# Kernel tuning notes

Hardware: AMD Instinct MI355X
Metric: run time of the kernel (lower is better)

The kernel has to match this reference:

```python
import jax, jax.numpy as jnp
import numpy as np

# Faithful distillation of AttentionNet's cross-modal attention block.
# The resnet50/PointNet backbones are replaced by their output feature maps
# (img: [B,256,64,64], pc2d: [B,2048,64,64]) supplied as inputs, since the
# kernel-relevant math is the conv1x1 projections + bmm/softmax/bmm attention,
# followed by global avg-pool, concat, and the fc + log_softmax head.
# Note: the original forward contains a bug (img_v1 overwritten by img.view)
# and dead code; we implement the clearly intended attention math.

B, CQ, CK, H, W = 16, 256, 2048, 64, 64
NUM_CLASS = 40


def conv1x1(x, w, b):
    # x: [B,Cin,H,W], w: [Cout,Cin], b: [Cout]
    return jnp.einsum('bchw,oc->bohw', x, w) + b[None, :, None, None]


def setup_inputs() -> dict:
    key = jax.random.key(0)
    ks = jax.random.split(key, 16)
    s = lambda fan_in: 1.0 / np.sqrt(fan_in)
    return {
        'img': jax.random.normal(ks[0], (B, CQ, H, W), jnp.float32),
        'pc2d': jax.random.normal(ks[1], (B, CK, H, W), jnp.float32),
        'Wq': jax.random.normal(ks[2], (CQ, CQ), jnp.float32) * s(CQ),
        'bq': jnp.zeros((CQ,), jnp.float32),
        'Wk': jax.random.normal(ks[3], (CQ, CK), jnp.float32) * s(CK),
        'bk': jnp.zeros((CQ,), jnp.float32),
        'Wvi': jax.random.normal(ks[4], (CQ, CQ), jnp.float32) * s(CQ),
        'bvi': jnp.zeros((CQ,), jnp.float32),
        'Wvp': jax.random.normal(ks[5], (CK, CK), jnp.float32) * s(CK),
        'bvp': jnp.zeros((CK,), jnp.float32),
        'gamma1': jnp.zeros((1,), jnp.float32),
        'W1': jax.random.normal(ks[6], (1024, CQ + CK), jnp.float32) * s(CQ + CK),
        'b1': jnp.zeros((1024,), jnp.float32),
        'W2': jax.random.normal(ks[7], (NUM_CLASS, 1024), jnp.float32) * s(1024),
        'b2': jnp.zeros((NUM_CLASS,), jnp.float32),
    }


def reference(img, pc2d, Wq, bq, Wk, bk, Wvi, bvi, Wvp, bvp, gamma1, W1, b1, W2, b2):
    N = H * W  # 4096
    q = conv1x1(img, Wq, bq).reshape(B, CQ, N).transpose(0, 2, 1)   # [B,N,256]
    k = conv1x1(pc2d, Wk, bk).reshape(B, CQ, N)                     # [B,256,N]
    att = jax.nn.softmax(jnp.einsum('bnc,bcm->bnm', q, k), axis=-1)  # [B,N,N]
    # image branch: out = gamma * bmm(V_img, att^T) + img
    vi = conv1x1(img, Wvi, bvi).reshape(B, CQ, N)
    img_att = jnp.einsum('bcn,bmn->bcm', vi, att).reshape(B, CQ, H, W)
    img_out = gamma1[0] * img_att + img
    # point-cloud branch: bmm(V_pc, att^T)
    vp = conv1x1(pc2d, Wvp, bvp).reshape(B, CK, N)
    pc_out = jnp.einsum('bcn,bmn->bcm', vp, att)                    # [B,2048,N]
    # global average pool + concat + MLP head with log_softmax
    img_feat = img_out.mean(axis=(2, 3))                            # [B,256]
    pc_feat = pc_out.mean(axis=2)                                   # [B,2048]
    fused = jnp.concatenate([img_feat, pc_feat], axis=-1)           # [B,2304]
    h = jax.nn.relu(fused @ W1.T + b1)
    logits = h @ W2.T + b2
    return jax.nn.log_softmax(logits, axis=1)
```

## Files before the change

### kernel.cpp

```cpp
#include <hip/hip_runtime.h>
#include <cstdint>

typedef __attribute__((ext_vector_type(8))) short short8;
typedef __attribute__((ext_vector_type(4))) float f32x4;

#define LOG2E 1.44269504088896340736f
#define SHIFT 64.0f

__device__ __forceinline__ unsigned short f2bf(float x) {
  union { float f; unsigned u; } c; c.f = x;
  unsigned r = c.u + 0x7fffu + ((c.u >> 16) & 1u);
  return (unsigned short)(r >> 16);
}

__device__ __forceinline__ void gl2lds16(const void* g, void* l) {
  __builtin_amdgcn_global_load_lds((const __attribute__((address_space(1))) void*)g,
                                   (__attribute__((address_space(3))) void*)l, 16, 0, 0);
}

__global__ void cvt_bf16(const float* __restrict__ src, unsigned short* __restrict__ dst, int n4) {
  int i = blockIdx.x * 256 + threadIdx.x;
  if (i >= n4) return;
  float4 v = ((const float4*)src)[i];
  ushort4 o;
  o.x = f2bf(v.x); o.y = f2bf(v.y); o.z = f2bf(v.z); o.w = f2bf(v.w);
  ((ushort4*)dst)[i] = o;
}

__device__ __forceinline__ void stage_resident(char* ldsbase, const char* src, int w, int lane) {
  const int p = lane & 31;
  const int rlo = lane >> 5;
#pragma unroll
  for (int it = 0; it < 16; ++it) {
    const int r = w * 32 + it * 2 + rlo;
    const int gs = (p & 24) | ((p & 7) ^ (r & 7));
    gl2lds16(src + (size_t)r * 512 + gs * 16, ldsbase + (w * 16 + it) * 1024);
  }
}

__device__ __forceinline__ void stage_stream(char* buf, const char* srcbase, int roff0, int roff1,
                                             int w) {
  gl2lds16(srcbase + roff0, buf + w * 1024);
  gl2lds16(srcbase + roff1, buf + 4096 + w * 1024);
}

__global__ __launch_bounds__(256, 2) void attn_rowsum(
    const unsigned short* __restrict__ qt, const unsigned short* __restrict__ kt,
    float* __restrict__ row_l) {
  extern __shared__ char pool[];
  const int b = blockIdx.y, i0 = blockIdx.x * 128;
  const int t = threadIdx.x, w = t >> 6, lane = t & 63, q = lane >> 4, ln = lane & 15;
  const int ihalf = w >> 1, jhalf = w & 1;
  const char* qres = (const char*)(qt + ((size_t)b * 4096 + i0) * 256);
  const char* kb = (const char*)(kt + (size_t)b * 4096 * 256);
  const int rr0 = w * 16 + (lane >> 2);
  const int gsS = (lane & 3) ^ ((lane >> 3) & 3);
  const int roff0 = rr0 * 512 + gsS * 16;
  const int roff1 = (64 + rr0) * 512 + gsS * 16;
  const int aRow = (ihalf * 64 + ln) * 512;
  const int bRow = jhalf * 4096 + ln * 64 + (q ^ ((ln >> 1) & 3)) * 16;
  float lacc[4][4] = {};

  stage_resident(pool, qres, w, lane);
  stage_stream(pool + 65536, kb, roff0, roff1, w);
  __syncthreads();

#pragma unroll 1
  for (int jt = 0; jt < 32; ++jt) {
    f32x4 acc[4][4] = {};
#pragma unroll
    for (int c = 0; c < 8; ++c) {
      const int s = jt * 8 + c;
      if (s + 1 < 256) {
        const int njt = (s + 1) >> 3, nc = (s + 1) & 7;
        stage_stream(pool + 65536 + ((s + 1) & 1) * 8192,
                     kb + (size_t)njt * 65536 + nc * 64, roff0, roff1, w);
      }
      const char* B = pool + 65536 + (s & 1) * 8192;
      const int posA = ((4 * c) & 24) | ((4 * (c & 1) + q) ^ (ln & 7));
      short8 af[4], bfr[4];
#pragma unroll
      for (int mt = 0; mt < 4; ++mt) af[mt] = *(const short8*)(pool + aRow + mt * 8192 + posA * 16);
#pragma unroll
      for (int nt = 0; nt < 4; ++nt) bfr[nt] = *(const short8*)(B + bRow + nt * 1024);
#pragma unroll
      for (int mt = 0; mt < 4; ++mt)
#pragma unroll
        for (int nt = 0; nt < 4; ++nt)
          acc[mt][nt] = __builtin_amdgcn_mfma_f32_16x16x32_bf16(af[mt], bfr[nt], acc[mt][nt], 0, 0, 0);
      __syncthreads();
    }
#pragma unroll
    for (int mt = 0; mt < 4; ++mt)
#pragma unroll
      for (int r = 0; r < 4; ++r) {
        float e = exp2f(acc[mt][0][r] * LOG2E - SHIFT) + exp2f(acc[mt][1][r] * LOG2E - SHIFT)
                + exp2f(acc[mt][2][r] * LOG2E - SHIFT) + exp2f(acc[mt][3][r] * LOG2E - SHIFT);
        e += __shfl_xor(e, 1); e += __shfl_xor(e, 2);
        e += __shfl_xor(e, 4); e += __shfl_xor(e, 8);
        lacc[mt][r] += e;
      }
  }
  float* lred = (float*)(pool + 65536);
  if (ln == 0) {
#pragma unroll
    for (int mt = 0; mt < 4; ++mt)
#pragma unroll
      for (int r = 0; r < 4; ++r)
        lred[jhalf * 128 + ihalf * 64 + mt * 16 + q * 4 + r] = lacc[mt][r];
  }
  __syncthreads();
  if (t < 128) row_l[b * 4096 + i0 + t] = lred[t] + lred[128 + t];
}

__global__ void inv_kernel(const float* __restrict__ l, float* __restrict__ linv) {
  int i = blockIdx.x * 256 + threadIdx.x;
  linv[i] = 1.0f / l[i];
}

__global__ __launch_bounds__(256, 2) void attn_colsum(
    const unsigned short* __restrict__ qt, const unsigned short* __restrict__ kt,
    const float* __restrict__ linv, float* __restrict__ s_col) {
  extern __shared__ char pool[];
  const int b = blockIdx.y, j0 = blockIdx.x * 128;
  const int t = threadIdx.x, w = t >> 6, lane = t & 63, q = lane >> 4, ln = lane & 15;
  const int ihalf = w >> 1, jhalf = w & 1;
  const char* kres = (const char*)(kt + ((size_t)b * 4096 + j0) * 256);
  const char* qb = (const char*)(qt + (size_t)b * 4096 * 256);
  const int rr0 = w * 16 + (lane >> 2);
  const int gsS = (lane & 3) ^ ((lane >> 3) & 3);
  const int roff0 = rr0 * 512 + gsS * 16;
  const int roff1 = (64 + rr0) * 512 + gsS * 16;
  const int aRow = ihalf * 4096 + ln * 64 + (q ^ ((ln >> 1) & 3)) * 16;
  const int bRow = (jhalf * 64 + ln) * 512;
  float scacc[4] = {};

  stage_resident(pool, kres, w, lane);
  stage_stream(pool + 65536, qb, roff0, roff1, w);
  __syncthreads();

#pragma unroll 1
  for (int it = 0; it < 32; ++it) {
    const float4* lp = (const float4*)(linv + (size_t)b * 4096 + it * 128 + ihalf * 64 + q * 4);
    float4 lv[4];
#pragma unroll
    for (int mt = 0; mt < 4; ++mt) lv[mt] = lp[mt * 4];

    f32x4 acc[4][4] = {};
#pragma unroll
    for (int c = 0; c < 8; ++c) {
      const int s = it * 8 + c;
      if (s + 1 < 256) {
        const int nit = (s + 1) >> 3, nc = (s + 1) & 7;
        stage_stream(pool + 65536 + ((s + 1) & 1) * 8192,
                     qb + (size_t)nit * 65536 + nc * 64, roff0, roff1, w);
      }
      const char* A = pool + 65536 + (s & 1) * 8192;
      const int posB = ((4 * c) & 24) | ((4 * (c & 1) + q) ^ (ln & 7));
      short8 af[4], bfr[4];
#pragma unroll
      for (int mt = 0; mt < 4; ++mt) af[mt] = *(const short8*)(A + aRow + mt * 1024);
#pragma unroll
      for (int nt = 0; nt < 4; ++nt) bfr[nt] = *(const short8*)(pool + bRow + nt * 8192 + posB * 16);
#pragma unroll
      for (int mt = 0; mt < 4; ++mt)
#pragma unroll
        for (int nt = 0; nt < 4; ++nt)
          acc[mt][nt] = __builtin_amdgcn_mfma_f32_16x16x32_bf16(af[mt], bfr[nt], acc[mt][nt], 0, 0, 0);
      __syncthreads();
    }
#pragma unroll
    for (int nt = 0; nt < 4; ++nt) {
      float v = 0.f;
#pragma unroll
      for (int mt = 0; mt < 4; ++mt) {
        v += exp2f(acc[mt][nt][0] * LOG2E - SHIFT) * lv[mt].x;
        v += exp2f(acc[mt][nt][1] * LOG2E - SHIFT) * lv[mt].y;
        v += exp2f(acc[mt][nt][2] * LOG2E - SHIFT) * lv[mt].z;
        v += exp2f(acc[mt][nt][3] * LOG2E - SHIFT) * lv[mt].w;
      }
      v += __shfl_xor(v, 16); v += __shfl_xor(v, 32);
      scacc[nt] += v;
    }
  }
  float* sred = (float*)(pool + 65536);
  if (q == 0) {
#pragma unroll
    for (int nt = 0; nt < 4; ++nt)
      sred[ihalf * 128 + jhalf * 64 + nt * 16 + ln] = scacc[nt];
  }
  __syncthreads();
  if (t < 128) s_col[b * 4096 + j0 + t] = sred[t] + sred[128 + t];
}

__global__ __launch_bounds__(256, 2) void proj_kernel(
    const float* __restrict__ In, const unsigned short* __restrict__ Wbf,
    const float* __restrict__ bias, unsigned short* __restrict__ Out, int Kdim) {
  __shared__ unsigned short Alds[64 * 72];
  __shared__ unsigned short Blds[256 * 72];
  const int b = blockIdx.y, sp0 = blockIdx.x * 64;
  const int t = threadIdx.x, w = t >> 6, lane = t & 63, q = lane >> 4, ln = lane & 15;
  f32x4 acc[4][4] = {};
  const int nch = Kdim >> 6;
  for (int ch = 0; ch < nch; ++ch) {
    const int ci0 = ch * 64;
#pragma unroll
    for (int p = 0; p < 8; ++p) {
      int s = t + 256 * p;
      int row = s >> 3, sl = s & 7;
      *(uint4*)(&Blds[row * 72 + sl * 8]) = *(const uint4*)(&Wbf[(size_t)row * Kdim + ci0 + sl * 8]);
    }
    {
      const int cp = t >> 3, spg = t & 7;
      const float* r0 = In + ((size_t)b * Kdim + ci0 + 2 * cp) * 4096 + sp0 + spg * 8;
      const float* r1 = r0 + 4096;
      float4 a0 = *(const float4*)(r0);
      float4 a1 = *(const float4*)(r0 + 4);
      float4 b0 = *(const float4*)(r1);
      float4 b1 = *(const float4*)(r1 + 4);
      float va[8] = {a0.x, a0.y, a0.z, a0.w, a1.x, a1.y, a1.z, a1.w};
      float vb[8] = {b0.x, b0.y, b0.z, b0.w, b1.x, b1.y, b1.z, b1.w};
#pragma unroll
      for (int k2 = 0; k2 < 8; ++k2) {
        unsigned u0 = f2bf(va[k2]), u1 = f2bf(vb[k2]);
        *(unsigned*)(&Alds[(spg * 8 + k2) * 72 + 2 * cp]) = u0 | (u1 << 16);
      }
    }
    __syncthreads();
#pragma unroll
    for (int ks = 0; ks < 2; ++ks) {
      short8 af[4], bfr[4];
#pragma unroll
      for (int mt = 0; mt < 4; ++mt)
        af[mt] = *(const short8*)(&Alds[(mt * 16 + ln) * 72 + ks * 32 + q * 8]);
#pragma unroll
      for (int nt = 0; nt < 4; ++nt)
        bfr[nt] = *(const short8*)(&Blds[(w * 64 + nt * 16 + ln) * 72 + ks * 32 + q * 8]);
#pragma unroll
      for (int mt = 0; mt < 4; ++mt)
#pragma unroll
        for (int nt = 0; nt < 4; ++nt)
          acc[mt][nt] = __builtin_amdgcn_mfma_f32_16x16x32_bf16(af[mt], bfr[nt], acc[mt][nt], 0, 0, 0);
    }
    __syncthreads();
  }
#pragma unroll
  for (int nt = 0; nt < 4; ++nt) {
    int co = w * 64 + nt * 16 + ln;
    float bv = bias[co];
#pragma unroll
    for (int mt = 0; mt < 4; ++mt)
#pragma unroll
      for (int r = 0; r < 4; ++r) {
        int sp = sp0 + mt * 16 + q * 4 + r;
        Out[((size_t)b * 4096 + sp) * 256 + co] = f2bf(acc[mt][nt][r] + bv);
      }
  }
}

__global__ void sbar_kernel(const float* __restrict__ s_col, float* __restrict__ sbar) {
  const int b = blockIdx.x, t = threadIdx.x;
  float v = 0.f;
  for (int k = 0; k < 16; ++k) v += s_col[b * 4096 + t + 256 * k];
  for (int m = 1; m < 64; m <<= 1) v += __shfl_xor(v, m);
  __shared__ float red[4];
  if ((t & 63) == 0) red[t >> 6] = v;
  __syncthreads();
  if (t == 0) sbar[b] = (red[0] + red[1] + red[2] + red[3]) * (1.f / 4096.f);
}

__global__ void pool_kernel(const float* __restrict__ img, const float* __restrict__ pc2d,
                            const float* __restrict__ s_col, float* __restrict__ u_pool,
                            float* __restrict__ imean, float* __restrict__ t_pool) {
  const int b = blockIdx.y, chunk = blockIdx.x;
  const int t = threadIdx.x, ch_l = t >> 2, j = t & 3;
  const bool isimg = chunk < 4;
  int ch;
  const float4* row4;
  if (isimg) {
    ch = chunk * 64 + ch_l;
    row4 = (const float4*)(img + ((size_t)b * 256 + ch) * 4096);
  } else {
    ch = (chunk - 4) * 64 + ch_l;
    row4 = (const float4*)(pc2d + ((size_t)b * 2048 + ch) * 4096);
  }
  const float4* s4 = (const float4*)(s_col + b * 4096);
  float accd = 0.f, accs = 0.f;
  for (int kk = 0; kk < 256; ++kk) {
    float4 x = row4[j + 4 * kk];
    float4 sv = s4[j + 4 * kk];
    accd += x.x * sv.x + x.y * sv.y + x.z * sv.z + x.w * sv.w;
    accs += x.x + x.y + x.z + x.w;
  }
  accd += __shfl_xor(accd, 1); accd += __shfl_xor(accd, 2);
  accs += __shfl_xor(accs, 1); accs += __shfl_xor(accs, 2);
  if (j == 0) {
    if (isimg) {
      u_pool[b * 256 + ch] = accd * (1.f / 4096.f);
      imean[b * 256 + ch] = accs * (1.f / 4096.f);
    } else {
      t_pool[b * 2048 + ch] = accd * (1.f / 4096.f);
    }
  }
}

__global__ void imgfeat_kernel(const float* __restrict__ Wvi, const float* __restrict__ bvi,
                               const float* __restrict__ gamma1, const float* __restrict__ u_pool,
                               const float* __restrict__ imean, const float* __restrict__ sbar,
                               float* __restrict__ fused) {
  const int t = threadIdx.x;
  const int co = blockIdx.x * 64 + (t >> 2), j = t & 3;
  float acc[16];
#pragma unroll
  for (int b = 0; b < 16; ++b) acc[b] = 0.f;
  const float4* w4 = (const float4*)(Wvi + (size_t)co * 256);
  for (int kk = 0; kk < 16; ++kk) {
    float4 wv = w4[j + 4 * kk];
#pragma unroll
    for (int b = 0; b < 16; ++b) {
      float4 uv = ((const float4*)(u_pool + b * 256))[j + 4 * kk];
      acc[b] += wv.x * uv.x + wv.y * uv.y + wv.z * uv.z + wv.w * uv.w;
    }
  }
#pragma unroll
  for (int b = 0; b < 16; ++b) { acc[b] += __shfl_xor(acc[b], 1); acc[b] += __shfl_xor(acc[b], 2); }
  if (j == 0) {
    float g = gamma1[0], bv = bvi[co];
#pragma unroll
    for (int b = 0; b < 16; ++b)
      fused[b * 2304 + co] = g * (acc[b] + bv * sbar[b]) + imean[b * 256 + co];
  }
}

__global__ void pcfeat_kernel(const float* __restrict__ Wvp, const float* __restrict__ bvp,
                              const float* __restrict__ t_pool, const float* __restrict__ sbar,
                              float* __restrict__ fused) {
  const int t = threadIdx.x;
  const int co = blockIdx.x * 64 + (t >> 2), j = t & 3;
  float acc[16];
#pragma unroll
  for (int b = 0; b < 16; ++b) acc[b] = 0.f;
  const float4* w4 = (const float4*)(Wvp + (size_t)co * 2048);
  for (int kk = 0; kk < 128; ++kk) {
    float4 wv = w4[j + 4 * kk];
#pragma unroll
    for (int b = 0; b < 16; ++b) {
      float4 tv = ((const float4*)(t_pool + b * 2048))[j + 4 * kk];
      acc[b] += wv.x * tv.x + wv.y * tv.y + wv.z * tv.z + wv.w * tv.w;
    }
  }
#pragma unroll
  for (int b = 0; b < 16; ++b) { acc[b] += __shfl_xor(acc[b], 1); acc[b] += __shfl_xor(acc[b], 2); }
  if (j == 0) {
    float bv = bvp[co];
#pragma unroll
    for (int b = 0; b < 16; ++b)
      fused[b * 2304 + 256 + co] = acc[b] + bv * sbar[b];
  }
}

__global__ void head1_kernel(const float* __restrict__ W1, const float* __restrict__ b1,
                             const float* __restrict__ fused, float* __restrict__ h) {
  const int t = threadIdx.x;
  const int o = blockIdx.x * 64 + (t >> 2), j = t & 3;
  float acc[16];
#pragma unroll
  for (int b = 0; b < 16; ++b) acc[b] = 0.f;
  const float4* w4 = (const float4*)(W1 + (size_t)o * 2304);
  for (int kk = 0; kk < 144; ++kk) {
    float4 wv = w4[j + 4 * kk];
#pragma unroll
    for (int b = 0; b < 16; ++b) {
      float4 fv = ((const float4*)(fused + b * 2304))[j + 4 * kk];
      acc[b] += wv.x * fv.x + wv.y * fv.y + wv.z * fv.z + wv.w * fv.w;
    }
  }
#pragma unroll
  for (int b = 0; b < 16; ++b) { acc[b] += __shfl_xor(acc[b], 1); acc[b] += __shfl_xor(acc[b], 2); }
  if (j == 0) {
    float bv = b1[o];
#pragma unroll
    for (int b = 0; b < 16; ++b) h[b * 1024 + o] = fmaxf(acc[b] + bv, 0.f);
  }
}

__global__ void head2_kernel(const float* __restrict__ W2, const float* __restrict__ b2,
                             const float* __restrict__ h, float* __restrict__ out) {
  const int b = blockIdx.x, t = threadIdx.x;
  __shared__ float logit[40];
  __shared__ float red[4];
  float4 hv = ((const float4*)(h + b * 1024))[t];
  for (int c = 0; c < 40; ++c) {
    float4 wv = ((const float4*)(W2 + (size_t)c * 1024))[t];
    float p = wv.x * hv.x + wv.y * hv.y + wv.z * hv.z + wv.w * hv.w;
    for (int m = 1; m < 64; m <<= 1) p += __shfl_xor(p, m);
    if ((t & 63) == 0) red[t >> 6] = p;
    __syncthreads();
    if (t == 0) logit[c] = red[0] + red[1] + red[2] + red[3] + b2[c];
    __syncthreads();
  }
  if (t == 0) {
    float mx = -1e30f;
    for (int c = 0; c < 40; ++c) mx = fmaxf(mx, logit[c]);
    float s = 0.f;
    for (int c = 0; c < 40; ++c) s += expf(logit[c] - mx);
    float ls = logf(s);
    for (int c = 0; c < 40; ++c) out[b * 40 + c] = logit[c] - mx - ls;
  }
}

extern "C" void kernel_launch(void* const* d_in, const int* in_sizes, int n_in,
                              void* d_out, int out_size, void* d_ws, size_t ws_size,
                              hipStream_t stream) {
  (void)in_sizes; (void)n_in; (void)out_size; (void)ws_size;
  const float* img    = (const float*)d_in[0];
  const float* pc2d   = (const float*)d_in[1];
  const float* Wq     = (const float*)d_in[2];
  const float* bq     = (const float*)d_in[3];
  const float* Wk     = (const float*)d_in[4];
  const float* bk     = (const float*)d_in[5];
  const float* Wvi    = (const float*)d_in[6];
  const float* bvi    = (const float*)d_in[7];
  const float* Wvp    = (const float*)d_in[8];
  const float* bvp    = (const float*)d_in[9];
  const float* gamma1 = (const float*)d_in[10];
  const float* W1     = (const float*)d_in[11];
  const float* b1     = (const float*)d_in[12];
  const float* W2     = (const float*)d_in[13];
  const float* b2     = (const float*)d_in[14];

  char* ws = (char*)d_ws;
  unsigned short* q_t   = (unsigned short*)(ws + 0);
  unsigned short* k_t   = (unsigned short*)(ws + 33554432);
  unsigned short* wq_bf = (unsigned short*)(ws + 67108864);
  unsigned short* wk_bf = (unsigned short*)(ws + 67239936);
  float* linv   = (float*)(ws + 68288512);
  float* row_l  = (float*)(ws + 68550656);
  float* s_col  = (float*)(ws + 68812800);
  float* sbar   = (float*)(ws + 69074944);
  float* u_pool = (float*)(ws + 69075008);
  float* imean  = (float*)(ws + 69091392);
  float* t_pool = (float*)(ws + 69107776);
  float* fusedb = (float*)(ws + 69238848);
  float* h_buf  = (float*)(ws + 69386304);

  hipFuncSetAttribute((const void*)attn_rowsum, hipFuncAttributeMaxDynamicSharedMemorySize, 81920);
  hipFuncSetAttribute((const void*)attn_colsum, hipFuncAttributeMaxDynamicSharedMemorySize, 81920);

  cvt_bf16<<<dim3(64), dim3(256), 0, stream>>>(Wq, wq_bf, 16384);
  cvt_bf16<<<dim3(512), dim3(256), 0, stream>>>(Wk, wk_bf, 131072);

  proj_kernel<<<dim3(64, 16), dim3(256), 0, stream>>>(img, wq_bf, bq, q_t, 256);
  proj_kernel<<<dim3(64, 16), dim3(256), 0, stream>>>(pc2d, wk_bf, bk, k_t, 2048);

  attn_rowsum<<<dim3(32, 16), dim3(256), 81920, stream>>>(q_t, k_t, row_l);
  inv_kernel<<<dim3(256), dim3(256), 0, stream>>>(row_l, linv);
  attn_colsum<<<dim3(32, 16), dim3(256), 81920, stream>>>(q_t, k_t, linv, s_col);

  sbar_kernel<<<dim3(16), dim3(256), 0, stream>>>(s_col, sbar);
  pool_kernel<<<dim3(36, 16), dim3(256), 0, stream>>>(img, pc2d, s_col, u_pool, imean, t_pool);

  imgfeat_kernel<<<dim3(4), dim3(256), 0, stream>>>(Wvi, bvi, gamma1, u_pool, imean, sbar, fusedb);
  pcfeat_kernel<<<dim3(32), dim3(256), 0, stream>>>(Wvp, bvp, t_pool, sbar, fusedb);

  head1_kernel<<<dim3(16), dim3(256), 0, stream>>>(W1, b1, fusedb, h_buf);
  head2_kernel<<<dim3(16), dim3(256), 0, stream>>>(W2, b2, h_buf, (float*)d_out);
}
```

Before: 1.650 ms.

## Enlarge projection tile to 128 spatial, load weights direct-to-LDS with swizzle

The conv1x1 projection kernel now handles 128 spatial positions per block instead of 64. This halves the number of weight-tile reloads per output, and each wave now computes a 64x128 sub-tile. Weight tiles go global-to-LDS through the async load path, and both LDS tiles use an XOR swizzle instead of padding to avoid bank conflicts. The cost is twice the accumulator registers per thread (128 floats) and half as many blocks, so occupancy and grid fill are at risk.

```diff
diff --git a/kernel.cpp b/kernel.cpp
--- a/kernel.cpp
+++ b/kernel.cpp
@@ -193,37 +193,49 @@
   if (t < 128) s_col[b * 4096 + j0 + t] = sred[t] + sred[128 + t];
 }
 
-__global__ __launch_bounds__(256, 2) void proj_kernel(
+__global__ __launch_bounds__(256, 2) void proj2_kernel(
     const float* __restrict__ In, const unsigned short* __restrict__ Wbf,
     const float* __restrict__ bias, unsigned short* __restrict__ Out, int Kdim) {
-  __shared__ unsigned short Alds[64 * 72];
-  __shared__ unsigned short Blds[256 * 72];
-  const int b = blockIdx.y, sp0 = blockIdx.x * 64;
+  __shared__ char Alds[128 * 144];
+  __shared__ char Blds[256 * 128];
+  const int b = blockIdx.y, sp0 = blockIdx.x * 128;
   const int t = threadIdx.x, w = t >> 6, lane = t & 63, q = lane >> 4, ln = lane & 15;
-  f32x4 acc[4][4] = {};
+  const int shalf = w >> 1;
+  const int cq = w & 1;
+  const size_t wrow = (size_t)Kdim * 2;
+  f32x4 acc[2][4][4] = {};
   const int nch = Kdim >> 6;
+
+  const int brow0 = w * 8 + (lane >> 3);
+  const int bgs = (lane & 7) ^ (lane >> 3);
+  const int cp = t >> 3;
+  const int spg = t & 7;
+
+#pragma unroll 1
   for (int ch = 0; ch < nch; ++ch) {
     const int ci0 = ch * 64;
-#pragma unroll
-    for (int p = 0; p < 8; ++p) {
-      int s = t + 256 * p;
-      int row = s >> 3, sl = s & 7;
-      *(uint4*)(&Blds[row * 72 + sl * 8]) = *(const uint4*)(&Wbf[(size_t)row * Kdim + ci0 + sl * 8]);
-    }
+    const char* wsrc = (const char*)Wbf + (size_t)ci0 * 2 + bgs * 16;
+#pragma unroll
+    for (int i = 0; i < 8; ++i)
+      gl2lds16(wsrc + (size_t)(brow0 + i * 32) * wrow, Blds + i * 4096 + w * 1024);
     {
-      const int cp = t >> 3, spg = t & 7;
-      const float* r0 = In + ((size_t)b * Kdim + ci0 + 2 * cp) * 4096 + sp0 + spg * 8;
+      const float* r0 = In + ((size_t)b * Kdim + ci0 + 2 * cp) * 4096 + sp0 + spg * 16;
       const float* r1 = r0 + 4096;
-      float4 a0 = *(const float4*)(r0);
-      float4 a1 = *(const float4*)(r0 + 4);
-      float4 b0 = *(const float4*)(r1);
-      float4 b1 = *(const float4*)(r1 + 4);
-      float va[8] = {a0.x, a0.y, a0.z, a0.w, a1.x, a1.y, a1.z, a1.w};
-      float vb[8] = {b0.x, b0.y, b0.z, b0.w, b1.x, b1.y, b1.z, b1.w};
-#pragma unroll
-      for (int k2 = 0; k2 < 8; ++k2) {
-        unsigned u0 = f2bf(va[k2]), u1 = f2bf(vb[k2]);
-        *(unsigned*)(&Alds[(spg * 8 + k2) * 72 + 2 * cp]) = u0 | (u1 << 16);
+#pragma unroll
+      for (int h = 0; h < 2; ++h) {
+        float4 a0 = *(const float4*)(r0 + h * 8);
+        float4 a1 = *(const float4*)(r0 + h * 8 + 4);
+        float4 b0 = *(const float4*)(r1 + h * 8);
+        float4 b1 = *(const float4*)(r1 + h * 8 + 4);
+        float va[8] = {a0.x, a0.y, a0.z, a0.w, a1.x, a1.y, a1.z, a1.w};
+        float vb[8] = {b0.x, b0.y, b0.z, b0.w, b1.x, b1.y, b1.z, b1.w};
+#pragma unroll
+        for (int e = 0; e < 8; ++e) {
+          const int spl = spg * 16 + h * 8 + e;
+          const int colb = (cp << 2) ^ (((spl >> 4) & 7) << 4);
+          unsigned u0 = f2bf(va[e]), u1 = f2bf(vb[e]);
+          *(unsigned*)(Alds + spl * 144 + colb) = u0 | (u1 << 16);
+        }
       }
     }
     __syncthreads();
@@ -231,31 +243,43 @@
     for (int ks = 0; ks < 2; ++ks) {
       short8 af[4], bfr[4];
 #pragma unroll
+      for (int mt = 0; mt < 4; ++mt) {
+        const int row = shalf * 64 + mt * 16 + ln;
+        const int colr = (ks * 64 + q * 16) ^ (((row >> 4) & 7) << 4);
+        af[mt] = *(const short8*)(Alds + row * 144 + colr);
+      }
+#pragma unroll
+      for (int cb = 0; cb < 2; ++cb) {
+#pragma unroll
+        for (int nt = 0; nt < 4; ++nt) {
+          const int row = cb * 128 + cq * 64 + nt * 16 + ln;
+          const int pos = (ks * 4 + q) ^ (ln & 7);
+          bfr[nt] = *(const short8*)(Blds + row * 128 + pos * 16);
+        }
+#pragma unroll
+        for (int mt = 0; mt < 4; ++mt)
+#pragma unroll
+          for (int nt = 0; nt < 4; ++nt)
+            acc[cb][mt][nt] =
+                __builtin_amdgcn_mfma_f32_16x16x32_bf16(af[mt], bfr[nt], acc[cb][mt][nt], 0, 0, 0);
+      }
+    }
+    __syncthreads();
+  }
+#pragma unroll
+  for (int cb = 0; cb < 2; ++cb)
+#pragma unroll
+    for (int nt = 0; nt < 4; ++nt) {
+      const int co = cb * 128 + cq * 64 + nt * 16 + ln;
+      const float bv = bias[co];
+#pragma unroll
       for (int mt = 0; mt < 4; ++mt)
-        af[mt] = *(const short8*)(&Alds[(mt * 16 + ln) * 72 + ks * 32 + q * 8]);
-#pragma unroll
-      for (int nt = 0; nt < 4; ++nt)
-        bfr[nt] = *(const short8*)(&Blds[(w * 64 + nt * 16 + ln) * 72 + ks * 32 + q * 8]);
-#pragma unroll
-      for (int mt = 0; mt < 4; ++mt)
-#pragma unroll
-        for (int nt = 0; nt < 4; ++nt)
-          acc[mt][nt] = __builtin_amdgcn_mfma_f32_16x16x32_bf16(af[mt], bfr[nt], acc[mt][nt], 0, 0, 0);
-    }
-    __syncthreads();
-  }
-#pragma unroll
-  for (int nt = 0; nt < 4; ++nt) {
-    int co = w * 64 + nt * 16 + ln;
-    float bv = bias[co];
-#pragma unroll
-    for (int mt = 0; mt < 4; ++mt)
-#pragma unroll
-      for (int r = 0; r < 4; ++r) {
-        int sp = sp0 + mt * 16 + q * 4 + r;
-        Out[((size_t)b * 4096 + sp) * 256 + co] = f2bf(acc[mt][nt][r] + bv);
-      }
-  }
+#pragma unroll
+        for (int r = 0; r < 4; ++r) {
+          const int sp = sp0 + shalf * 64 + mt * 16 + q * 4 + r;
+          Out[((size_t)b * 4096 + sp) * 256 + co] = f2bf(acc[cb][mt][nt][r] + bv);
+        }
+    }
 }
 
 __global__ void sbar_kernel(const float* __restrict__ s_col, float* __restrict__ sbar) {
@@ -450,8 +474,8 @@
   cvt_bf16<<<dim3(64), dim3(256), 0, stream>>>(Wq, wq_bf, 16384);
   cvt_bf16<<<dim3(512), dim3(256), 0, stream>>>(Wk, wk_bf, 131072);
 
-  proj_kernel<<<dim3(64, 16), dim3(256), 0, stream>>>(img, wq_bf, bq, q_t, 256);
-  proj_kernel<<<dim3(64, 16), dim3(256), 0, stream>>>(pc2d, wk_bf, bk, k_t, 2048);
+  proj2_kernel<<<dim3(32, 16), dim3(256), 0, stream>>>(img, wq_bf, bq, q_t, 256);
+  proj2_kernel<<<dim3(32, 16), dim3(256), 0, stream>>>(pc2d, wk_bf, bk, k_t, 2048);
 
   attn_rowsum<<<dim3(32, 16), dim3(256), 81920, stream>>>(q_t, k_t, row_l);
   inv_kernel<<<dim3(256), dim3(256), 0, stream>>>(row_l, linv);
```

Measured after the change: 1.622 ms. Within noise of the previous version (-1.7%).
